# Kernel optimization log

Measured on AMD Instinct MI355X. Metric: run time of the kernel, lower is better.

## Reference

```python
import jax, jax.numpy as jnp
import numpy as np

B, T, C = 2, 2048, 2048
H, HD = 16, 128  # num_heads, head_dim; inner_dim = H*HD = C
EPS = 1e-8


def _hadamard(n):
    # Sylvester construction, orthonormal scaling 1/sqrt(n)
    h = np.array([[1.0]], dtype=np.float32)
    while h.shape[0] < n:
        h = np.block([[h, h], [h, -h]])
    return jnp.asarray(h / np.sqrt(n), dtype=jnp.float32)


def _round_ste(x):
    # straight-through rounding (matches int8 training-time quantization semantics)
    return x + jax.lax.stop_gradient(jnp.round(x) - x)


def q8_linear(x, w):
    # dynamic per-token int8 activation quant + per-out-channel int8 weight quant
    s_x = jnp.max(jnp.abs(x), axis=-1, keepdims=True) / 127.0 + EPS   # (B,T,1)
    xq = _round_ste(jnp.clip(x / s_x, -127.0, 127.0))
    s_w = jnp.max(jnp.abs(w), axis=-1, keepdims=True) / 127.0 + EPS   # (O,1)
    wq = _round_ste(jnp.clip(w / s_w, -127.0, 127.0))
    return jnp.einsum('btk,ok->bto', xq, wq) * s_x * s_w[:, 0]


def rmsnorm(x, g, eps=1e-6):
    return x * jax.lax.rsqrt(jnp.mean(x * x, axis=-1, keepdims=True) + eps) * g


def apply_rope(x, cos, sin):
    # x: (B,T,H*HD); cos/sin: (T,HD/2); interleaved rotary per head
    b, t, c = x.shape
    xh = x.reshape(b, t, -1, HD)
    x1, x2 = xh[..., 0::2], xh[..., 1::2]
    co = cos[None, :, None, :]
    si = sin[None, :, None, :]
    o1 = x1 * co - x2 * si
    o2 = x1 * si + x2 * co
    out = jnp.stack([o1, o2], axis=-1).reshape(b, t, -1, HD)
    return out.reshape(b, t, c)


def setup_inputs() -> dict:
    key = jax.random.key(0)
    ks = jax.random.split(key, 8)
    hidden_states = jax.random.normal(ks[0], (B, T, C), jnp.float32)
    attention_mask = jax.random.randint(ks[1], (B,), 1, T + 1).astype(jnp.int32)  # valid lengths
    sc = 1.0 / np.sqrt(C)
    wq = jax.random.normal(ks[2], (H * HD, C), jnp.float32) * sc
    wk = jax.random.normal(ks[3], (H * HD, C), jnp.float32) * sc
    wv = jax.random.normal(ks[4], (H * HD, C), jnp.float32) * sc
    wo = jax.random.normal(ks[5], (C, H * HD), jnp.float32) * (1.0 / np.sqrt(H * HD))
    q_gamma = jnp.ones((H * HD,), jnp.float32)
    k_gamma = jnp.ones((H * HD,), jnp.float32)
    inv_freq = 1.0 / (10000.0 ** (np.arange(0, HD, 2, dtype=np.float32) / HD))
    freqs = np.outer(np.arange(T, dtype=np.float32), inv_freq)  # (T, HD/2)
    cos = jnp.asarray(np.cos(freqs), jnp.float32)
    sin = jnp.asarray(np.sin(freqs), jnp.float32)
    return {"hidden_states": hidden_states, "attention_mask": attention_mask,
            "wq": wq, "wk": wk, "wv": wv, "wo": wo,
            "q_gamma": q_gamma, "k_gamma": k_gamma, "cos": cos, "sin": sin}


def reference(hidden_states, attention_mask, wq, wk, wv, wo, q_gamma, k_gamma, cos, sin):
    b, t, c = hidden_states.shape
    q = rmsnorm(q8_linear(hidden_states, wq), q_gamma)
    k = rmsnorm(q8_linear(hidden_states, wk), k_gamma)
    v = q8_linear(hidden_states, wv)
    q = apply_rope(q, cos, sin)
    k = apply_rope(k, cos, sin)
    # (B,T,H*HD) -> (B,H,T,HD)
    q = q.reshape(b, t, H, HD).transpose(0, 2, 1, 3)
    k = k.reshape(b, t, H, HD).transpose(0, 2, 1, 3)
    v = v.reshape(b, t, H, HD).transpose(0, 2, 1, 3)
    # Hadamard rotation of q/k head dims (orthonormal -> preserves qk dot products)
    Hm = _hadamard(HD)
    qh = q @ Hm
    kh = k @ Hm
    scores = jnp.einsum('bhqd,bhkd->bhqk', qh, kh) * (1.0 / np.sqrt(HD))
    # ragged batch mask: keys beyond per-batch valid length are masked out
    valid = jnp.arange(t)[None, :] < attention_mask[:, None]   # (B,T)
    scores = jnp.where(valid[:, None, None, :], scores, -1e9)
    p = jax.nn.softmax(scores, axis=-1)
    o = jnp.einsum('bhqk,bhkd->bhqd', p, v)
    o = o.transpose(0, 2, 1, 3).reshape(b, t, c)
    return q8_linear(o, wo)
```

## Files before the change

### kernel.cpp

```cpp
#include <hip/hip_runtime.h>
#include <stdint.h>

typedef unsigned short u16;
typedef unsigned int u32;
typedef int v4i __attribute__((ext_vector_type(4)));
typedef float v4f __attribute__((ext_vector_type(4)));
typedef short v8s __attribute__((ext_vector_type(8)));

#define Bn 2
#define Tn 2048
#define Cn 2048
#define Hn 16
#define HDn 128

__device__ __forceinline__ float b2f(u16 u) {
    u32 x = ((u32)u) << 16;
    float f;
    __builtin_memcpy(&f, &x, 4);
    return f;
}
__device__ __forceinline__ u16 f2b(float f) {
    u32 x;
    __builtin_memcpy(&x, &f, 4);
    u32 r = (x + 0x7fffu + ((x >> 16) & 1u)) >> 16;
    return (u16)r;
}

__device__ __forceinline__ void async16(const void* g, void* l) {
    __builtin_amdgcn_global_load_lds(
        (const __attribute__((address_space(1))) u32*)g,
        (__attribute__((address_space(3))) u32*)l, 16, 0, 0);
}

__global__ __launch_bounds__(256) void quant_all(
    const float* __restrict__ w0, const float* __restrict__ w1,
    const float* __restrict__ w2, const float* __restrict__ w3,
    const float* __restrict__ hid, int8_t* __restrict__ Q,
    float* __restrict__ S) {
    int r = blockIdx.x;
    const float* src;
    int ro;
    if (r < 2048) { src = w0; ro = r; }
    else if (r < 4096) { src = w1; ro = r - 2048; }
    else if (r < 6144) { src = w2; ro = r - 4096; }
    else if (r < 8192) { src = w3; ro = r - 6144; }
    else { src = hid; ro = r - 8192; }
    const float* x = src + (size_t)ro * Cn;
    int tid = threadIdx.x;
    float4 v0 = ((const float4*)x)[tid * 2];
    float4 v1 = ((const float4*)x)[tid * 2 + 1];
    float a[8] = {v0.x, v0.y, v0.z, v0.w, v1.x, v1.y, v1.z, v1.w};
    float m = 0.f;
#pragma unroll
    for (int i = 0; i < 8; i++) m = fmaxf(m, fabsf(a[i]));
#pragma unroll
    for (int o = 32; o; o >>= 1) m = fmaxf(m, __shfl_xor(m, o));
    __shared__ float sm[4];
    if ((tid & 63) == 0) sm[tid >> 6] = m;
    __syncthreads();
    m = fmaxf(fmaxf(sm[0], sm[1]), fmaxf(sm[2], sm[3]));
    float s = m * (1.0f / 127.0f) + 1e-8f;
    if (tid == 0) S[r] = s;
    u32 lo = 0, hi = 0;
#pragma unroll
    for (int i = 0; i < 8; i++) {
        float q = rintf(fminf(127.f, fmaxf(-127.f, a[i] / s)));
        int qi = (int)q;
        u32 byte = (u32)(qi & 0xff);
        if (i < 4) lo |= byte << (8 * i);
        else hi |= byte << (8 * (i - 4));
    }
    u32* qp = (u32*)(Q + (size_t)r * Cn);
    qp[tid * 2] = lo;
    qp[tid * 2 + 1] = hi;
}

__global__ __launch_bounds__(256) void quant_rows(const float* __restrict__ X,
                                                  int8_t* __restrict__ Q,
                                                  float* __restrict__ S) {
    int r = blockIdx.x;
    const float* x = X + (size_t)r * Cn;
    int tid = threadIdx.x;
    float4 v0 = ((const float4*)x)[tid * 2];
    float4 v1 = ((const float4*)x)[tid * 2 + 1];
    float a[8] = {v0.x, v0.y, v0.z, v0.w, v1.x, v1.y, v1.z, v1.w};
    float m = 0.f;
#pragma unroll
    for (int i = 0; i < 8; i++) m = fmaxf(m, fabsf(a[i]));
#pragma unroll
    for (int o = 32; o; o >>= 1) m = fmaxf(m, __shfl_xor(m, o));
    __shared__ float sm[4];
    if ((tid & 63) == 0) sm[tid >> 6] = m;
    __syncthreads();
    m = fmaxf(fmaxf(sm[0], sm[1]), fmaxf(sm[2], sm[3]));
    float s = m * (1.0f / 127.0f) + 1e-8f;
    if (tid == 0) S[r] = s;
    u32 lo = 0, hi = 0;
#pragma unroll
    for (int i = 0; i < 8; i++) {
        float q = rintf(fminf(127.f, fmaxf(-127.f, a[i] / s)));
        int qi = (int)q;
        u32 byte = (u32)(qi & 0xff);
        if (i < 4) lo |= byte << (8 * i);
        else hi |= byte << (8 * (i - 4));
    }
    u32* qp = (u32*)(Q + (size_t)r * Cn);
    qp[tid * 2] = lo;
    qp[tid * 2 + 1] = hi;
}

__global__ __launch_bounds__(256) void gemm_i8(
    const int8_t* __restrict__ A, const int8_t* __restrict__ Bw,
    const float* __restrict__ sA, const float* __restrict__ sB,
    void* __restrict__ Co, long long bStride, long long sbStride,
    long long cStride, int fp32out) {
    int z = blockIdx.z;
    Bw += (size_t)z * bStride;
    sB += (size_t)z * sbStride;
    const int K = 2048, N = 2048;
    __shared__ int8_t As[128 * 64];
    __shared__ int8_t Bs[128 * 64];
    int m0 = blockIdx.x * 128, n0 = blockIdx.y * 128;
    int tid = threadIdx.x, w = tid >> 6, lane = tid & 63;
    int quad = lane >> 4, l15 = lane & 15;
    int wy = w >> 1, wx = w & 1;
    const v4i zi = {0, 0, 0, 0};
    v4i acc[4][4];
#pragma unroll
    for (int i = 0; i < 4; i++)
#pragma unroll
        for (int j = 0; j < 4; j++) acc[i][j] = zi;
    int lrow = lane >> 2;
    int slot = lane & 3;
    int srow = w * 32 + lrow;
    int klog = ((slot ^ (lrow & 3)) * 16);
    const int8_t* ga = A + (size_t)(m0 + srow) * K + klog;
    const int8_t* gb = Bw + (size_t)(n0 + srow) * K + klog;
    int8_t* la = &As[srow * 64 + slot * 16];
    int8_t* lb = &Bs[srow * 64 + slot * 16];
    for (int k0 = 0; k0 < K; k0 += 64) {
        async16(ga + k0, la);
        async16(ga + k0 + (size_t)16 * K, la + 16 * 64);
        async16(gb + k0, lb);
        async16(gb + k0 + (size_t)16 * K, lb + 16 * 64);
        __syncthreads();
        int swz = (quad ^ (l15 & 3)) * 16;
        v4i af[4], bf4[4];
#pragma unroll
        for (int i = 0; i < 4; i++)
            af[i] = *(const v4i*)&As[(wy * 64 + i * 16 + l15) * 64 + swz];
#pragma unroll
        for (int j = 0; j < 4; j++)
            bf4[j] = *(const v4i*)&Bs[(wx * 64 + j * 16 + l15) * 64 + swz];
#pragma unroll
        for (int i = 0; i < 4; i++)
#pragma unroll
            for (int j = 0; j < 4; j++)
                acc[i][j] = __builtin_amdgcn_mfma_i32_16x16x64_i8(
                    af[i], bf4[j], acc[i][j], 0, 0, 0);
        __syncthreads();
    }
#pragma unroll
    for (int i = 0; i < 4; i++) {
        int mb = m0 + wy * 64 + i * 16 + quad * 4;
        float s0 = sA[mb], s1 = sA[mb + 1], s2 = sA[mb + 2], s3 = sA[mb + 3];
#pragma unroll
        for (int j = 0; j < 4; j++) {
            int n = n0 + wx * 64 + j * 16 + l15;
            float sb = sB[n];
            if (fp32out) {
                float* cp = (float*)Co + (size_t)cStride * z + (size_t)mb * N + n;
                cp[0] = (float)acc[i][j][0] * s0 * sb;
                cp[N] = (float)acc[i][j][1] * s1 * sb;
                cp[2 * N] = (float)acc[i][j][2] * s2 * sb;
                cp[3 * N] = (float)acc[i][j][3] * s3 * sb;
            } else {
                u16* cp = (u16*)Co + (size_t)cStride * z + (size_t)mb * N + n;
                cp[0] = f2b((float)acc[i][j][0] * s0 * sb);
                cp[N] = f2b((float)acc[i][j][1] * s1 * sb);
                cp[2 * N] = f2b((float)acc[i][j][2] * s2 * sb);
                cp[3 * N] = f2b((float)acc[i][j][3] * s3 * sb);
            }
        }
    }
}

__global__ __launch_bounds__(256) void norm_rope2(u16* __restrict__ Qb,
                                                  u16* __restrict__ Kb,
                                                  const float* __restrict__ qg,
                                                  const float* __restrict__ kg,
                                                  const float* __restrict__ cs,
                                                  const float* __restrict__ sn) {
    int row = blockIdx.x;
    int isq = row < 4096;
    row &= 4095;
    u16* x = (isq ? Qb : Kb) + (size_t)row * Cn;
    const float* g = isq ? qg : kg;
    float ps = isq ? 0.08838834764831845f : 1.0f;
    int t = row & (Tn - 1);
    int tid = threadIdx.x;
    uint4 raw = ((const uint4*)x)[tid];
    u16 us[8];
    us[0] = raw.x & 0xffff; us[1] = raw.x >> 16;
    us[2] = raw.y & 0xffff; us[3] = raw.y >> 16;
    us[4] = raw.z & 0xffff; us[5] = raw.z >> 16;
    us[6] = raw.w & 0xffff; us[7] = raw.w >> 16;
    float v[8];
#pragma unroll
    for (int i = 0; i < 8; i++) v[i] = b2f(us[i]);
    float ss = 0.f;
#pragma unroll
    for (int i = 0; i < 8; i++) ss += v[i] * v[i];
#pragma unroll
    for (int o = 32; o; o >>= 1) ss += __shfl_xor(ss, o);
    __shared__ float sm[4];
    if ((tid & 63) == 0) sm[tid >> 6] = ss;
    __syncthreads();
    ss = sm[0] + sm[1] + sm[2] + sm[3];
    float r = rsqrtf(ss * (1.f / 2048.f) + 1e-6f) * ps;
    float4 g0 = ((const float4*)g)[tid * 2];
    float4 g1 = ((const float4*)g)[tid * 2 + 1];
    float n[8];
    n[0] = v[0] * r * g0.x; n[1] = v[1] * r * g0.y;
    n[2] = v[2] * r * g0.z; n[3] = v[3] * r * g0.w;
    n[4] = v[4] * r * g1.x; n[5] = v[5] * r * g1.y;
    n[6] = v[6] * r * g1.z; n[7] = v[7] * r * g1.w;
    int pi = (tid & 15) * 4;
    float4 c4 = *(const float4*)(cs + t * 64 + pi);
    float4 s4 = *(const float4*)(sn + t * 64 + pi);
    float o[8];
    o[0] = n[0] * c4.x - n[1] * s4.x; o[1] = n[0] * s4.x + n[1] * c4.x;
    o[2] = n[2] * c4.y - n[3] * s4.y; o[3] = n[2] * s4.y + n[3] * c4.y;
    o[4] = n[4] * c4.z - n[5] * s4.z; o[5] = n[4] * s4.z + n[5] * c4.z;
    o[6] = n[6] * c4.w - n[7] * s4.w; o[7] = n[6] * s4.w + n[7] * c4.w;
    uint4 out;
    out.x = (u32)f2b(o[0]) | ((u32)f2b(o[1]) << 16);
    out.y = (u32)f2b(o[2]) | ((u32)f2b(o[3]) << 16);
    out.z = (u32)f2b(o[4]) | ((u32)f2b(o[5]) << 16);
    out.w = (u32)f2b(o[6]) | ((u32)f2b(o[7]) << 16);
    ((uint4*)x)[tid] = out;
}

__global__ __launch_bounds__(256) void vtrans(const u16* __restrict__ V,
                                              u16* __restrict__ Vt) {
    int bh = blockIdx.y;
    int b = bh >> 4, h = bh & 15;
    int t0 = blockIdx.x * 64;
    __shared__ u32 tile[64][133];
    int tid = threadIdx.x;
    int r = tid >> 2, seg = (tid & 3) * 32;
    const uint4* src =
        (const uint4*)(V + ((size_t)b * Tn + t0 + r) * Cn + h * HDn + seg);
#pragma unroll
    for (int i = 0; i < 4; i++) {
        uint4 u = src[i];
        u32 uu[4] = {u.x, u.y, u.z, u.w};
#pragma unroll
        for (int j = 0; j < 4; j++) {
            tile[r][seg + i * 8 + j * 2] = uu[j] & 0xffff;
            tile[r][seg + i * 8 + j * 2 + 1] = uu[j] >> 16;
        }
    }
    __syncthreads();
    int d = tid >> 1, tseg = (tid & 1) * 32;
    u16* dst = Vt + ((size_t)bh * HDn + d) * Tn + t0 + tseg;
#pragma unroll
    for (int i = 0; i < 4; i++) {
        u32 p0 = tile[tseg + i * 8 + 0][d] | (tile[tseg + i * 8 + 1][d] << 16);
        u32 p1 = tile[tseg + i * 8 + 2][d] | (tile[tseg + i * 8 + 3][d] << 16);
        u32 p2 = tile[tseg + i * 8 + 4][d] | (tile[tseg + i * 8 + 5][d] << 16);
        u32 p3 = tile[tseg + i * 8 + 6][d] | (tile[tseg + i * 8 + 7][d] << 16);
        ((uint4*)dst)[i] = make_uint4(p0, p1, p2, p3);
    }
}

__global__ __launch_bounds__(256, 2) void flash(const u16* __restrict__ Qb,
                                                const u16* __restrict__ Kb,
                                                const u16* __restrict__ Vt,
                                                const int* __restrict__ mask,
                                                float* __restrict__ O) {
    int qt = blockIdx.x, bh = blockIdx.y;
    int b = bh >> 4, h = bh & 15;
    int L = mask[b];
    int nkfull = L >> 6;
    int nk = (L + 63) >> 6;
    __shared__ u16 Ks[2][64 * 128];
    __shared__ u16 Vs[2][128 * 64];
    __shared__ u16 Ps[64 * 72];
    __shared__ float sred[256];
    __shared__ float sinv[64];
    int tid = threadIdx.x, w = tid >> 6, lane = tid & 63;
    int quad = lane >> 4, l15 = lane & 15;

    v8s aq[4][4];
#pragma unroll
    for (int i = 0; i < 4; i++)
#pragma unroll
        for (int kk = 0; kk < 4; kk++)
            aq[i][kk] = *(const v8s*)(Qb +
                                      ((size_t)b * Tn + qt * 64 + i * 16 + l15) * Cn +
                                      h * HDn + kk * 32 + quad * 8);

    const u16* ksp[4];
    const u16* vsp[4];
    int kdo[4], vdo[4];
#pragma unroll
    for (int cc = 0; cc < 4; cc++) {
        int c = w * 4 + cc;
        int rk = c * 4 + (lane >> 4);
        int sk = lane & 15;
        int lgk = sk ^ (rk & 7);
        ksp[cc] = Kb + ((size_t)b * Tn + rk) * Cn + h * HDn + lgk * 8;
        kdo[cc] = rk * 128 + sk * 8;
        int rv = c * 8 + (lane >> 3);
        int sv = lane & 7;
        int lgv = sv ^ (rv & 7);
        vsp[cc] = Vt + ((size_t)bh * HDn + rv) * Tn + lgv * 8;
        vdo[cc] = rv * 64 + sv * 8;
    }

    float sum16[16];
#pragma unroll
    for (int j = 0; j < 16; j++) sum16[j] = 0.f;
    const v4f zf = {0.f, 0.f, 0.f, 0.f};
    v4f oacc[4][2];
#pragma unroll
    for (int m = 0; m < 4; m++) {
        oacc[m][0] = zf;
        oacc[m][1] = zf;
    }

#pragma unroll
    for (int cc = 0; cc < 4; cc++) {
        async16(ksp[cc], &Ks[0][kdo[cc]]);
        async16(vsp[cc], &Vs[0][vdo[cc]]);
        ksp[cc] += (size_t)64 * Cn;
        vsp[cc] += 64;
    }

    int cur = 0;
    for (int kt = 0; kt < nk; kt++) {
        __syncthreads();
        if (kt + 1 < nk) {
#pragma unroll
            for (int cc = 0; cc < 4; cc++) {
                async16(ksp[cc], &Ks[cur ^ 1][kdo[cc]]);
                async16(vsp[cc], &Vs[cur ^ 1][vdo[cc]]);
                ksp[cc] += (size_t)64 * Cn;
                vsp[cc] += 64;
            }
        }
        v4f sacc[4] = {zf, zf, zf, zf};
        const u16* krow = &Ks[cur][(w * 16 + l15) * 128];
#pragma unroll
        for (int kk = 0; kk < 4; kk++) {
            v8s bk = *(const v8s*)(krow + ((((kk * 4 + quad) ^ (l15 & 7))) << 3));
#pragma unroll
            for (int i = 0; i < 4; i++)
                sacc[i] = __builtin_amdgcn_mfma_f32_16x16x32_bf16(aq[i][kk], bk,
                                                                  sacc[i], 0, 0, 0);
        }
        bool valid = (kt < nkfull) || ((kt * 64 + w * 16 + l15) < L);
#pragma unroll
        for (int i = 0; i < 4; i++)
#pragma unroll
            for (int r2 = 0; r2 < 4; r2++) {
                float p = valid ? __expf(sacc[i][r2]) : 0.f;
                sum16[i * 4 + r2] += p;
                Ps[(i * 16 + quad * 4 + r2) * 72 + w * 16 + l15] = f2b(p);
            }
        __syncthreads();
#pragma unroll
        for (int kk2 = 0; kk2 < 2; kk2++) {
            v8s ap[4];
#pragma unroll
            for (int m = 0; m < 4; m++)
                ap[m] = *(const v8s*)(Ps + (m * 16 + l15) * 72 + kk2 * 32 + quad * 8);
#pragma unroll
            for (int nbi = 0; nbi < 2; nbi++) {
                int vr = (2 * w + nbi) * 16 + l15;
                v8s bv = *(const v8s*)(&Vs[cur][vr * 64 +
                                       ((((kk2 * 4 + quad) ^ (l15 & 7))) << 3)]);
#pragma unroll
                for (int m = 0; m < 4; m++)
                    oacc[m][nbi] = __builtin_amdgcn_mfma_f32_16x16x32_bf16(
                        ap[m], bv, oacc[m][nbi], 0, 0, 0);
            }
        }
        cur ^= 1;
    }
#pragma unroll
    for (int j = 0; j < 16; j++) {
        float s = sum16[j];
        s += __shfl_xor(s, 1);
        s += __shfl_xor(s, 2);
        s += __shfl_xor(s, 4);
        s += __shfl_xor(s, 8);
        sum16[j] = s;
    }
    if (l15 == 0) {
#pragma unroll
        for (int i = 0; i < 4; i++)
#pragma unroll
            for (int r2 = 0; r2 < 4; r2++)
                sred[w * 64 + i * 16 + quad * 4 + r2] = sum16[i * 4 + r2];
    }
    __syncthreads();
    if (tid < 64)
        sinv[tid] =
            1.f / (sred[tid] + sred[64 + tid] + sred[128 + tid] + sred[192 + tid]);
    __syncthreads();
#pragma unroll
    for (int m = 0; m < 4; m++)
#pragma unroll
        for (int r2 = 0; r2 < 4; r2++) {
            float inv = sinv[m * 16 + quad * 4 + r2];
            int row = qt * 64 + m * 16 + quad * 4 + r2;
#pragma unroll
            for (int nbi = 0; nbi < 2; nbi++) {
                int d = h * HDn + (2 * w + nbi) * 16 + l15;
                O[((size_t)b * Tn + row) * Cn + d] = oacc[m][nbi][r2] * inv;
            }
        }
}

extern "C" void kernel_launch(void* const* d_in, const int* in_sizes, int n_in,
                              void* d_out, int out_size, void* d_ws,
                              size_t ws_size, hipStream_t stream) {
    const float* hidden = (const float*)d_in[0];
    const int* mask = (const int*)d_in[1];
    const float* wq = (const float*)d_in[2];
    const float* wk = (const float*)d_in[3];
    const float* wv = (const float*)d_in[4];
    const float* wo = (const float*)d_in[5];
    const float* qg = (const float*)d_in[6];
    const float* kg = (const float*)d_in[7];
    const float* cs = (const float*)d_in[8];
    const float* sn = (const float*)d_in[9];

    char* ws = (char*)d_ws;
    int8_t* q8 = (int8_t*)(ws);
    float* sAll = (float*)(ws + 25165824);
    u16* qb = (u16*)(ws + 25214976);
    u16* kb = (u16*)(ws + 41992192);
    u16* vb = (u16*)(ws + 58769408);
    u16* vt = (u16*)(ws + 75546624);
    float* Obuf = (float*)(ws + 92323840);
    int8_t* hid8 = q8 + 16777216;
    float* sx = sAll + 8192;

    quant_all<<<12288, 256, 0, stream>>>(wq, wk, wv, wo, hidden, q8, sAll);

    gemm_i8<<<dim3(32, 16, 3), 256, 0, stream>>>(hid8, q8, sx, sAll, (void*)qb,
                                                 4194304LL, 2048LL, 8388608LL, 0);

    norm_rope2<<<8192, 256, 0, stream>>>(qb, kb, qg, kg, cs, sn);
    vtrans<<<dim3(32, 32), 256, 0, stream>>>(vb, vt);

    flash<<<dim3(32, 32), 256, 0, stream>>>(qb, kb, vt, mask, Obuf);

    quant_rows<<<4096, 256, 0, stream>>>(Obuf, hid8, sx);
    gemm_i8<<<dim3(32, 16, 1), 256, 0, stream>>>(hid8, q8 + 12582912, sx,
                                                 sAll + 6144, d_out, 0LL, 0LL,
                                                 0LL, 1);
}
```

Baseline: 343.5 us.

## Load V fragments directly from global into registers in flash attention

The V tile is no longer staged through LDS with async copies. Each wave reads its transposed-V MFMA operands straight from global memory into registers. P is double-buffered in LDS so one barrier per iteration can be dropped, and the launch bounds rise to three blocks per CU because the LDS footprint shrinks. This removes LDS traffic and a barrier, but the V loads are now synchronous global reads issued each iteration with no prefetch, so their latency may be exposed. The higher occupancy target may also constrain registers.

```diff
diff --git a/kernel.cpp b/kernel.cpp
--- a/kernel.cpp
+++ b/kernel.cpp
@@ -274,7 +274,7 @@
     }
 }
 
-__global__ __launch_bounds__(256, 2) void flash(const u16* __restrict__ Qb,
+__global__ __launch_bounds__(256, 3) void flash(const u16* __restrict__ Qb,
                                                 const u16* __restrict__ Kb,
                                                 const u16* __restrict__ Vt,
                                                 const int* __restrict__ mask,
@@ -285,8 +285,7 @@
     int nkfull = L >> 6;
     int nk = (L + 63) >> 6;
     __shared__ u16 Ks[2][64 * 128];
-    __shared__ u16 Vs[2][128 * 64];
-    __shared__ u16 Ps[64 * 72];
+    __shared__ u16 Ps[2][64 * 72];
     __shared__ float sred[256];
     __shared__ float sinv[64];
     int tid = threadIdx.x, w = tid >> 6, lane = tid & 63;
@@ -302,8 +301,7 @@
                                       h * HDn + kk * 32 + quad * 8);
 
     const u16* ksp[4];
-    const u16* vsp[4];
-    int kdo[4], vdo[4];
+    int kdo[4];
 #pragma unroll
     for (int cc = 0; cc < 4; cc++) {
         int c = w * 4 + cc;
@@ -312,12 +310,10 @@
         int lgk = sk ^ (rk & 7);
         ksp[cc] = Kb + ((size_t)b * Tn + rk) * Cn + h * HDn + lgk * 8;
         kdo[cc] = rk * 128 + sk * 8;
-        int rv = c * 8 + (lane >> 3);
-        int sv = lane & 7;
-        int lgv = sv ^ (rv & 7);
-        vsp[cc] = Vt + ((size_t)bh * HDn + rv) * Tn + lgv * 8;
-        vdo[cc] = rv * 64 + sv * 8;
-    }
+    }
+
+    const u16* vp0 = Vt + ((size_t)bh * HDn + 2 * w * 16 + l15) * Tn + quad * 8;
+    const u16* vp1 = vp0 + 16 * Tn;
 
     float sum16[16];
 #pragma unroll
@@ -333,23 +329,25 @@
 #pragma unroll
     for (int cc = 0; cc < 4; cc++) {
         async16(ksp[cc], &Ks[0][kdo[cc]]);
-        async16(vsp[cc], &Vs[0][vdo[cc]]);
         ksp[cc] += (size_t)64 * Cn;
-        vsp[cc] += 64;
-    }
+    }
+    __syncthreads();
 
     int cur = 0;
     for (int kt = 0; kt < nk; kt++) {
-        __syncthreads();
         if (kt + 1 < nk) {
 #pragma unroll
             for (int cc = 0; cc < 4; cc++) {
                 async16(ksp[cc], &Ks[cur ^ 1][kdo[cc]]);
-                async16(vsp[cc], &Vs[cur ^ 1][vdo[cc]]);
                 ksp[cc] += (size_t)64 * Cn;
-                vsp[cc] += 64;
             }
         }
+        v8s bv00 = *(const v8s*)(vp0);
+        v8s bv10 = *(const v8s*)(vp0 + 32);
+        v8s bv01 = *(const v8s*)(vp1);
+        v8s bv11 = *(const v8s*)(vp1 + 32);
+        vp0 += 64;
+        vp1 += 64;
         v4f sacc[4] = {zf, zf, zf, zf};
         const u16* krow = &Ks[cur][(w * 16 + l15) * 128];
 #pragma unroll
@@ -367,7 +365,7 @@
             for (int r2 = 0; r2 < 4; r2++) {
                 float p = valid ? __expf(sacc[i][r2]) : 0.f;
                 sum16[i * 4 + r2] += p;
-                Ps[(i * 16 + quad * 4 + r2) * 72 + w * 16 + l15] = f2b(p);
+                Ps[cur][(i * 16 + quad * 4 + r2) * 72 + w * 16 + l15] = f2b(p);
             }
         __syncthreads();
 #pragma unroll
@@ -375,16 +373,16 @@
             v8s ap[4];
 #pragma unroll
             for (int m = 0; m < 4; m++)
-                ap[m] = *(const v8s*)(Ps + (m * 16 + l15) * 72 + kk2 * 32 + quad * 8);
-#pragma unroll
-            for (int nbi = 0; nbi < 2; nbi++) {
-                int vr = (2 * w + nbi) * 16 + l15;
-                v8s bv = *(const v8s*)(&Vs[cur][vr * 64 +
-                                       ((((kk2 * 4 + quad) ^ (l15 & 7))) << 3)]);
-#pragma unroll
-                for (int m = 0; m < 4; m++)
-                    oacc[m][nbi] = __builtin_amdgcn_mfma_f32_16x16x32_bf16(
-                        ap[m], bv, oacc[m][nbi], 0, 0, 0);
+                ap[m] = *(const v8s*)(&Ps[cur][(m * 16 + l15) * 72 + kk2 * 32 +
+                                               quad * 8]);
+            v8s bva = kk2 ? bv10 : bv00;
+            v8s bvb = kk2 ? bv11 : bv01;
+#pragma unroll
+            for (int m = 0; m < 4; m++) {
+                oacc[m][0] = __builtin_amdgcn_mfma_f32_16x16x32_bf16(
+                    ap[m], bva, oacc[m][0], 0, 0, 0);
+                oacc[m][1] = __builtin_amdgcn_mfma_f32_16x16x32_bf16(
+                    ap[m], bvb, oacc[m][1], 0, 0, 0);
             }
         }
         cur ^= 1;
```

New measurement: 340.1 us. No clear change (-1.0%).
